# Kernel tuning notes

Hardware: AMD Instinct MI355X
Metric: run time of the kernel (lower is better)

Reference implementation:

```python
import jax, jax.numpy as jnp
import numpy as np
from jax import lax

N, E = 100000, 1600000
IN_DIM, EDGE_DIM, HIDDEN, LAYERS, HEADS, OUT_DIM = 16, 4, 128, 6, 8, 3
C = HIDDEN // HEADS  # per-head dim
EPS = 1e-5


def setup_inputs() -> dict:
    key = jax.random.key(0)
    ks = jax.random.split(key, 24)
    s = 0.1
    inp = {
        "x": jax.random.normal(ks[0], (N, IN_DIM), jnp.float32),
        "edge_index": jax.random.randint(ks[1], (2, E), 0, N, jnp.int32),
        "edge_attr": jax.random.normal(ks[2], (E, EDGE_DIM), jnp.float32),
        # input projection
        "W_in": s * jax.random.normal(ks[3], (IN_DIM, HIDDEN), jnp.float32),
        "b_in": jnp.zeros((HIDDEN,), jnp.float32),
        "ln_in_g": jnp.ones((HIDDEN,), jnp.float32),
        "ln_in_b": jnp.zeros((HIDDEN,), jnp.float32),
        # stacked GAT layer params [L, ...]
        "Wg": s * jax.random.normal(ks[4], (LAYERS, HIDDEN, HIDDEN), jnp.float32),
        "att_src": s * jax.random.normal(ks[5], (LAYERS, HEADS, C), jnp.float32),
        "att_dst": s * jax.random.normal(ks[6], (LAYERS, HEADS, C), jnp.float32),
        "We": s * jax.random.normal(ks[7], (LAYERS, EDGE_DIM, HIDDEN), jnp.float32),
        "att_edge": s * jax.random.normal(ks[8], (LAYERS, HEADS, C), jnp.float32),
        "bg": jnp.zeros((LAYERS, HIDDEN), jnp.float32),
        "ln_g": jnp.ones((LAYERS, HIDDEN), jnp.float32),
        "ln_b": jnp.zeros((LAYERS, HIDDEN), jnp.float32),
        # output head
        "W1": s * jax.random.normal(ks[9], (HIDDEN, HIDDEN), jnp.float32),
        "b1": jnp.zeros((HIDDEN,), jnp.float32),
        "W2": s * jax.random.normal(ks[10], (HIDDEN, OUT_DIM), jnp.float32),
        "b2": jnp.zeros((OUT_DIM,), jnp.float32),
    }
    return inp


def layer_norm(x, g, b):
    mu = jnp.mean(x, axis=-1, keepdims=True)
    var = jnp.var(x, axis=-1, keepdims=True)
    return (x - mu) * lax.rsqrt(var + EPS) * g + b


def gat_block(h, src, dst, edge_attr, Wg, a_s, a_d, We, a_e, bg, g, b):
    # linear projection, shared for src/dst (same input set in PyG GATConv)
    hp = (h @ Wg).reshape(N, HEADS, C)                  # [N,H,C]
    alpha_src = jnp.sum(hp * a_s, axis=-1)              # [N,H]
    alpha_dst = jnp.sum(hp * a_d, axis=-1)              # [N,H]
    ep = (edge_attr @ We).reshape(E, HEADS, C)          # [E,H,C]
    alpha_e = jnp.sum(ep * a_e, axis=-1)                # [E,H]
    # edge-wise attention logits, leaky_relu slope 0.2 (PyG default)
    alpha = jax.nn.leaky_relu(alpha_src[src] + alpha_dst[dst] + alpha_e, 0.2)
    # segment softmax over incoming edges of each dst node
    m = jax.ops.segment_max(alpha, dst, num_segments=N)  # [N,H]
    m = jnp.where(jnp.isfinite(m), m, 0.0)
    a = jnp.exp(alpha - m[dst])
    denom = jax.ops.segment_sum(a, dst, num_segments=N)  # [N,H]
    a = a / (denom[dst] + 1e-16)
    # weighted message aggregation
    msg = hp[src] * a[:, :, None]                        # [E,H,C]
    out = jax.ops.segment_sum(msg, dst, num_segments=N).reshape(N, HIDDEN) + bg
    # residual + LayerNorm (dropout inactive in eval)
    return layer_norm(h + out, g, b)


def reference(x, edge_index, edge_attr, W_in, b_in, ln_in_g, ln_in_b,
              Wg, att_src, att_dst, We, att_edge, bg, ln_g, ln_b,
              W1, b1, W2, b2):
    src, dst = edge_index[0], edge_index[1]
    h = layer_norm(jax.nn.relu(x @ W_in + b_in), ln_in_g, ln_in_b)

    def body(h, p):
        Wg_i, as_i, ad_i, We_i, ae_i, bg_i, g_i, b_i = p
        return gat_block(h, src, dst, edge_attr, Wg_i, as_i, ad_i, We_i, ae_i, bg_i, g_i, b_i), None

    h, _ = lax.scan(body, h, (Wg, att_src, att_dst, We, att_edge, bg, ln_g, ln_b))
    h = jax.nn.relu(h @ W1 + b1)
    return jax.nn.relu(h @ W2 + b2)
```

## Files before the change

kernel.cpp:

```cpp
#include <hip/hip_runtime.h>
#include <hip/hip_bf16.h>

#define NN 100000
#define NE 1600000
#define HID 128
#define NH 8
#define HC 16
#define NL 6
#define CAP 64

typedef unsigned int u32;

__device__ __forceinline__ float u2f(unsigned short v){
  union{u32 i; float f;} c; c.i = ((u32)v) << 16; return c.f;
}
__device__ __forceinline__ float lo2f(u32 u){ union{u32 i; float f;} c; c.i = u << 16; return c.f; }
__device__ __forceinline__ float hi2f(u32 u){ union{u32 i; float f;} c; c.i = u & 0xFFFF0000u; return c.f; }
__device__ __forceinline__ unsigned short f2bf(float f){
  u32 u = __float_as_uint(f);
  u = (u + 0x7FFFu + ((u >> 16) & 1u)) >> 16;
  return (unsigned short)u;
}

__device__ __forceinline__ float ldw(const void* p, long long i, int fl){
  if (fl) return ((const float*)p)[i];
  return u2f(((const unsigned short*)p)[i]);
}

__global__ void sniff_k(const void* g, int* flag){
  if (threadIdx.x == 0 && blockIdx.x == 0){
    const unsigned short* p = (const unsigned short*)g;
    flag[0] = (p[0] == 0x3F80) ? 0 : 1;
  }
}

__global__ void zero_k(int* p, int n){
  int i = blockIdx.x*256 + threadIdx.x;
  if (i < n) p[i] = 0;
}

#define PF_TOT 4355
__global__ void prep_params_k(const void* att_src, const void* att_dst,
    const void* bg, const void* ln_g, const void* ln_b, const void* b1,
    const void* W2, const void* b2, float* __restrict__ pf, const int* flag){
  int fl = flag[0];
  int i = blockIdx.x*256 + threadIdx.x;
  if (i >= PF_TOT) return;
  float v;
  if (i < 768)       v = ldw(att_src, i, fl);
  else if (i < 1536) v = ldw(att_dst, i-768, fl);
  else if (i < 2304) v = ldw(bg, i-1536, fl);
  else if (i < 3072) v = ldw(ln_g, i-2304, fl);
  else if (i < 3840) v = ldw(ln_b, i-3072, fl);
  else if (i < 3968) v = ldw(b1, i-3840, fl);
  else if (i < 4352) v = ldw(W2, i-3968, fl);
  else               v = ldw(b2, i-4352, fl);
  pf[i] = v;
}

__global__ __launch_bounds__(256) void prep_wf_k(const void* Wg, const void* W1,
    float* __restrict__ wF, const int* flag){
  int fl = flag[0];
  long long i = (long long)blockIdx.x*256 + threadIdx.x;
  if (i >= (long long)7*HID*HID) return;
  float v = (i < (long long)6*HID*HID) ? ldw(Wg, i, fl) : ldw(W1, i - (long long)6*HID*HID, fl);
  wF[i] = v;
}

__global__ void prep_wae_k(const void* We, const void* ae, float* __restrict__ Wae,
                           const int* flag){
  int fl = flag[0];
  int id = threadIdx.x;
  if (id >= NL*4*NH) return;
  int l = id / 32, r = id % 32, d = r / 8, hh = r % 8;
  float s = 0.f;
  #pragma unroll
  for (int c = 0; c < HC; ++c)
    s += ldw(We, l*4*HID + d*HID + hh*HC + c, fl) * ldw(ae, l*NH*HC + hh*HC + c, fl);
  Wae[id] = s;
}

__global__ __launch_bounds__(256) void inproj_k(const void* x,
    const void* W_in, const void* b_in, const void* g, const void* b,
    float* __restrict__ h, const int* flag){
  __shared__ float xs[2][16];
  __shared__ float r1[2][2], r2[2][2];
  int fl = flag[0];
  int half = threadIdx.x >> 7;
  int t = threadIdx.x & 127;
  long long n = (long long)blockIdx.x*2 + half;
  if (t < 16) xs[half][t] = ldw(x, n*16 + t, fl);
  __syncthreads();
  float acc = ldw(b_in, t, fl);
  #pragma unroll
  for (int k = 0; k < 16; ++k) acc = fmaf(xs[half][k], ldw(W_in, k*HID + t, fl), acc);
  acc = fmaxf(acc, 0.f);
  float s1 = acc, s2 = acc*acc;
  #pragma unroll
  for (int off = 32; off; off >>= 1){ s1 += __shfl_xor(s1, off); s2 += __shfl_xor(s2, off); }
  if ((t & 63) == 0){ r1[half][t>>6] = s1; r2[half][t>>6] = s2; }
  __syncthreads();
  float S1 = r1[half][0] + r1[half][1], S2 = r2[half][0] + r2[half][1];
  float mu = S1 * (1.f/128.f);
  float var = S2 * (1.f/128.f) - mu*mu;
  float rr = rsqrtf(var + 1e-5f);
  h[n*HID + t] = (acc - mu) * rr * ldw(g, t, fl) + ldw(b, t, fl);
}

__global__ __launch_bounds__(256) void count_k(const int* __restrict__ dst,
    int* __restrict__ deg, int* __restrict__ pos){
  int e = blockIdx.x*256 + threadIdx.x;
  if (e >= NE) return;
  pos[e] = atomicAdd(&deg[dst[e]], 1);
}
__global__ __launch_bounds__(256) void scan_block_k(const int* __restrict__ in,
    int* __restrict__ out, int* __restrict__ bsum, int n){
  __shared__ int lds[256];
  int t = threadIdx.x, i = blockIdx.x*256 + t;
  int v = (i < n) ? in[i] : 0;
  lds[t] = v;
  __syncthreads();
  #pragma unroll
  for (int off = 1; off < 256; off <<= 1){
    int tmp = (t >= off) ? lds[t-off] : 0;
    __syncthreads();
    lds[t] += tmp;
    __syncthreads();
  }
  int incl = lds[t];
  if (i < n) out[i] = incl - v;
  if (t == 255) bsum[blockIdx.x] = incl;
}
__global__ __launch_bounds__(512) void scan_top_k(const int* __restrict__ bsum,
    int* __restrict__ boff, int nb){
  __shared__ int lds[512];
  int t = threadIdx.x;
  int v = (t < nb) ? bsum[t] : 0;
  lds[t] = v;
  __syncthreads();
  #pragma unroll
  for (int off = 1; off < 512; off <<= 1){
    int tmp = (t >= off) ? lds[t-off] : 0;
    __syncthreads();
    lds[t] += tmp;
    __syncthreads();
  }
  boff[t] = lds[t] - v;
}
__global__ __launch_bounds__(256) void scan_add_k(int* __restrict__ rowptr,
    const int* __restrict__ boff, int n){
  int i = blockIdx.x*256 + threadIdx.x;
  if (i < n) rowptr[i] += boff[i >> 8];
  if (i == 0) rowptr[n] = NE;
}
__global__ __launch_bounds__(256) void scatter_k(const int* __restrict__ src,
    const int* __restrict__ dst, const int* __restrict__ rowptr,
    const int* __restrict__ pos, const void* eattr,
    uint4* __restrict__ pk, const int* flag){
  int fl = flag[0];
  int e = blockIdx.x*256 + threadIdx.x;
  if (e >= NE) return;
  int d = dst[e];
  int i = rowptr[d] + pos[e];
  uint4 o;
  o.x = (u32)src[e];
  if (fl){
    float4 v = *(const float4*)((const float*)eattr + (long long)e*4);
    o.y = ((u32)f2bf(v.y) << 16) | (u32)f2bf(v.x);
    o.z = ((u32)f2bf(v.w) << 16) | (u32)f2bf(v.z);
  } else {
    uint2 er = *(const uint2*)((const unsigned short*)eattr + (long long)e*4);
    o.y = er.x; o.z = er.y;
  }
  o.w = 0;
  pk[i] = o;
}

__global__ __launch_bounds__(256) void gemm128_k(const float* __restrict__ A,
    const float* __restrict__ WF, unsigned short* __restrict__ Cout,
    const float* __restrict__ biasF, int relu,
    const float* __restrict__ attS, const float* __restrict__ attD,
    float* __restrict__ asrc, float* __restrict__ adst){
  __shared__ float At[32][132];
  __shared__ float Wt[32][132];
  int t = threadIdx.x;
  int row0 = blockIdx.x * 128;
  int tx = t & 15, ty = t >> 4;
  float acc[8][8] = {};
  for (int k0 = 0; k0 < 128; k0 += 32){
    int ar = t >> 1, ak = (t & 1) * 16;
    float a16[16];
    int arow = row0 + ar;
    if (arow < NN){
      const float* ap = A + (long long)arow*HID + k0 + ak;
      float4 q0 = *(const float4*)ap, q1 = *(const float4*)(ap+4);
      float4 q2 = *(const float4*)(ap+8), q3 = *(const float4*)(ap+12);
      a16[0]=q0.x; a16[1]=q0.y; a16[2]=q0.z; a16[3]=q0.w;
      a16[4]=q1.x; a16[5]=q1.y; a16[6]=q1.z; a16[7]=q1.w;
      a16[8]=q2.x; a16[9]=q2.y; a16[10]=q2.z; a16[11]=q2.w;
      a16[12]=q3.x; a16[13]=q3.y; a16[14]=q3.z; a16[15]=q3.w;
    } else {
      #pragma unroll
      for (int j = 0; j < 16; ++j) a16[j] = 0.f;
    }
    int wk = t >> 3, wn = (t & 7) * 16;
    float w16[16];
    {
      const float* wp = WF + (long long)(k0 + wk)*HID + wn;
      float4 q0 = *(const float4*)wp, q1 = *(const float4*)(wp+4);
      float4 q2 = *(const float4*)(wp+8), q3 = *(const float4*)(wp+12);
      w16[0]=q0.x; w16[1]=q0.y; w16[2]=q0.z; w16[3]=q0.w;
      w16[4]=q1.x; w16[5]=q1.y; w16[6]=q1.z; w16[7]=q1.w;
      w16[8]=q2.x; w16[9]=q2.y; w16[10]=q2.z; w16[11]=q2.w;
      w16[12]=q3.x; w16[13]=q3.y; w16[14]=q3.z; w16[15]=q3.w;
    }
    __syncthreads();
    #pragma unroll
    for (int j = 0; j < 16; ++j) At[ak+j][ar] = a16[j];
    #pragma unroll
    for (int j = 0; j < 16; j += 4){
      float4 q; q.x=w16[j]; q.y=w16[j+1]; q.z=w16[j+2]; q.w=w16[j+3];
      *(float4*)&Wt[wk][wn+j] = q;
    }
    __syncthreads();
    #pragma unroll
    for (int kk = 0; kk < 32; ++kk){
      float4 a0 = *(const float4*)&At[kk][ty*8];
      float4 a1 = *(const float4*)&At[kk][ty*8+4];
      float4 b0 = *(const float4*)&Wt[kk][tx*4];
      float4 b1 = *(const float4*)&Wt[kk][64 + tx*4];
      float am[8] = {a0.x,a0.y,a0.z,a0.w,a1.x,a1.y,a1.z,a1.w};
      float bn[8] = {b0.x,b0.y,b0.z,b0.w,b1.x,b1.y,b1.z,b1.w};
      #pragma unroll
      for (int i2 = 0; i2 < 8; ++i2){
        #pragma unroll
        for (int j2 = 0; j2 < 8; ++j2)
          acc[i2][j2] = fmaf(am[i2], bn[j2], acc[i2][j2]);
      }
    }
  }
  float bb[8];
  #pragma unroll
  for (int j2 = 0; j2 < 8; ++j2){
    int col = (j2 < 4) ? tx*4 + j2 : 64 + tx*4 + (j2 - 4);
    bb[j2] = biasF ? biasF[col] : 0.f;
  }
  #pragma unroll
  for (int i2 = 0; i2 < 8; ++i2){
    int row = row0 + ty*8 + i2;
    if (row < NN){
      float o[8];
      #pragma unroll
      for (int j2 = 0; j2 < 8; ++j2){
        float v = acc[i2][j2] + bb[j2];
        o[j2] = relu ? fmaxf(v, 0.f) : v;
      }
      uint2 p0, p1;
      p0.x = ((u32)f2bf(o[1]) << 16) | (u32)f2bf(o[0]);
      p0.y = ((u32)f2bf(o[3]) << 16) | (u32)f2bf(o[2]);
      p1.x = ((u32)f2bf(o[5]) << 16) | (u32)f2bf(o[4]);
      p1.y = ((u32)f2bf(o[7]) << 16) | (u32)f2bf(o[6]);
      *(uint2*)(Cout + (long long)row*HID + tx*4) = p0;
      *(uint2*)(Cout + (long long)row*HID + 64 + tx*4) = p1;
    }
  }
  if (attS){
    float (*pas)[8][4] = (float (*)[8][4])&At[0][0];
    float (*pad)[8][4] = (float (*)[8][4])&Wt[0][0];
    float avS[8], avD[8];
    #pragma unroll
    for (int j2 = 0; j2 < 8; ++j2){
      int col = (j2 < 4) ? tx*4 + j2 : 64 + tx*4 + (j2 - 4);
      avS[j2] = attS[col]; avD[j2] = attD[col];
    }
    int h0 = tx >> 2, slot = tx & 3;
    __syncthreads();
    #pragma unroll
    for (int i2 = 0; i2 < 8; ++i2){
      float ps0 = 0.f, pd0 = 0.f, ps1 = 0.f, pd1 = 0.f;
      #pragma unroll
      for (int j2 = 0; j2 < 4; ++j2){
        ps0 = fmaf(acc[i2][j2],   avS[j2],   ps0);
        pd0 = fmaf(acc[i2][j2],   avD[j2],   pd0);
        ps1 = fmaf(acc[i2][j2+4], avS[j2+4], ps1);
        pd1 = fmaf(acc[i2][j2+4], avD[j2+4], pd1);
      }
      int row = ty*8 + i2;
      pas[row][h0][slot] = ps0;   pad[row][h0][slot] = pd0;
      pas[row][h0+4][slot] = ps1; pad[row][h0+4][slot] = pd1;
    }
    __syncthreads();
    #pragma unroll
    for (int q = 0; q < 4; ++q){
      int idx = t + 256*q;
      int row = idx >> 3, hh = idx & 7;
      int rr = row0 + row;
      if (rr < NN){
        asrc[(long long)rr*NH + hh] = pas[row][hh][0] + pas[row][hh][1]
                                    + pas[row][hh][2] + pas[row][hh][3];
        adst[(long long)rr*NH + hh] = pad[row][hh][0] + pad[row][hh][1]
                                    + pad[row][hh][2] + pad[row][hh][3];
      }
    }
  }
}

__global__ __launch_bounds__(256) void gat_node_k(const int* __restrict__ rowptr,
    const uint4* __restrict__ pk,
    const float* __restrict__ Wae_l, const float* __restrict__ asrc,
    const float* __restrict__ adst, const unsigned short* __restrict__ hp,
    float* __restrict__ h, const float* __restrict__ bgF,
    const float* __restrict__ gF, const float* __restrict__ bF){
  __shared__ float lw[4][CAP][8];
  __shared__ int   ls[4][CAP];
  int wv = threadIdx.x >> 6, l = threadIdx.x & 63;
  int n = blockIdx.x*4 + wv;
  int b0 = rowptr[n], b1 = rowptr[n+1];
  int deg = b1 - b0;
  int sub = l >> 3, hh = l & 7;
  float wae0 = Wae_l[hh], wae1 = Wae_l[8+hh], wae2 = Wae_l[16+hh], wae3 = Wae_l[24+hh];
  float adn = adst[n*NH + hh];
  float den = 0.f;
  for (int i = b0 + sub; i < b1; i += 8){
    uint4 q = pk[i];
    int s = (int)q.x;
    float v = asrc[s*NH + hh] + adn;
    v = fmaf(lo2f(q.y), wae0, v);
    v = fmaf(hi2f(q.y), wae1, v);
    v = fmaf(lo2f(q.z), wae2, v);
    v = fmaf(hi2f(q.z), wae3, v);
    v = fmaxf(v, 0.2f*v);
    float w = __expf(v);
    int idx = i - b0;
    if (idx < CAP){
      lw[wv][idx][hh] = w;
      if (hh == 0) ls[wv][idx] = s;
    }
    den += w;
  }
  den += __shfl_xor(den, 8);
  den += __shfl_xor(den, 16);
  den += __shfl_xor(den, 32);
  int eg = l >> 4, cl = l & 15;
  int hd = cl >> 1;
  float rden = 1.f / (__shfl(den, hd) + 1e-16f);
  const unsigned short* hpc = hp + 8*cl;
  float a[8] = {0,0,0,0,0,0,0,0};
  int cap_end = b0 + (deg < CAP ? deg : CAP);
  int i = b0;
  for (; i + 8 <= cap_end; i += 8){
    int j0 = i + eg, j1 = i + 4 + eg;
    int s0 = ls[wv][j0 - b0], s1v = ls[wv][j1 - b0];
    float w0 = lw[wv][j0 - b0][hd], w1 = lw[wv][j1 - b0][hd];
    uint4 q0 = *(const uint4*)(hpc + (long long)s0*HID);
    uint4 q1 = *(const uint4*)(hpc + (long long)s1v*HID);
    a[0] = fmaf(w0, lo2f(q0.x), a[0]); a[1] = fmaf(w0, hi2f(q0.x), a[1]);
    a[2] = fmaf(w0, lo2f(q0.y), a[2]); a[3] = fmaf(w0, hi2f(q0.y), a[3]);
    a[4] = fmaf(w0, lo2f(q0.z), a[4]); a[5] = fmaf(w0, hi2f(q0.z), a[5]);
    a[6] = fmaf(w0, lo2f(q0.w), a[6]); a[7] = fmaf(w0, hi2f(q0.w), a[7]);
    a[0] = fmaf(w1, lo2f(q1.x), a[0]); a[1] = fmaf(w1, hi2f(q1.x), a[1]);
    a[2] = fmaf(w1, lo2f(q1.y), a[2]); a[3] = fmaf(w1, hi2f(q1.y), a[3]);
    a[4] = fmaf(w1, lo2f(q1.z), a[4]); a[5] = fmaf(w1, hi2f(q1.z), a[5]);
    a[6] = fmaf(w1, lo2f(q1.w), a[6]); a[7] = fmaf(w1, hi2f(q1.w), a[7]);
  }
  for (; i < cap_end; i += 4){
    int j = i + eg;
    if (j < cap_end){
      int s = ls[wv][j - b0];
      float w = lw[wv][j - b0][hd];
      uint4 q = *(const uint4*)(hpc + (long long)s*HID);
      a[0] = fmaf(w, lo2f(q.x), a[0]); a[1] = fmaf(w, hi2f(q.x), a[1]);
      a[2] = fmaf(w, lo2f(q.y), a[2]); a[3] = fmaf(w, hi2f(q.y), a[3]);
      a[4] = fmaf(w, lo2f(q.z), a[4]); a[5] = fmaf(w, hi2f(q.z), a[5]);
      a[6] = fmaf(w, lo2f(q.w), a[6]); a[7] = fmaf(w, hi2f(q.w), a[7]);
    }
  }
  if (deg > CAP){
    float w0c = Wae_l[hd], w1c = Wae_l[8+hd], w2c = Wae_l[16+hd], w3c = Wae_l[24+hd];
    float adc = adst[n*NH + hd];
    for (int j = cap_end + eg; j < b1; j += 4){
      uint4 e4 = pk[j];
      int s = (int)e4.x;
      float v = asrc[s*NH + hd] + adc;
      v = fmaf(lo2f(e4.y), w0c, v);
      v = fmaf(hi2f(e4.y), w1c, v);
      v = fmaf(lo2f(e4.z), w2c, v);
      v = fmaf(hi2f(e4.z), w3c, v);
      v = fmaxf(v, 0.2f*v);
      float w = __expf(v);
      uint4 q = *(const uint4*)(hpc + (long long)s*HID);
      a[0] = fmaf(w, lo2f(q.x), a[0]); a[1] = fmaf(w, hi2f(q.x), a[1]);
      a[2] = fmaf(w, lo2f(q.y), a[2]); a[3] = fmaf(w, hi2f(q.y), a[3]);
      a[4] = fmaf(w, lo2f(q.z), a[4]); a[5] = fmaf(w, hi2f(q.z), a[5]);
      a[6] = fmaf(w, lo2f(q.w), a[6]); a[7] = fmaf(w, hi2f(q.w), a[7]);
    }
  }
  #pragma unroll
  for (int j = 0; j < 8; ++j){
    a[j] += __shfl_xor(a[j], 16);
    a[j] += __shfl_xor(a[j], 32);
  }
  const float* hrow = h + (long long)n*HID + 8*cl;
  float4 hv0 = *(const float4*)hrow;
  float4 hv1 = *(const float4*)(hrow + 4);
  float hv[8] = {hv0.x,hv0.y,hv0.z,hv0.w,hv1.x,hv1.y,hv1.z,hv1.w};
  float tv[8];
  float s1 = 0.f, s2 = 0.f;
  #pragma unroll
  for (int j = 0; j < 8; ++j){
    tv[j] = hv[j] + a[j]*rden + bgF[8*cl + j];
    s1 += tv[j]; s2 += tv[j]*tv[j];
  }
  s1 += __shfl_xor(s1, 1); s2 += __shfl_xor(s2, 1);
  s1 += __shfl_xor(s1, 2); s2 += __shfl_xor(s2, 2);
  s1 += __shfl_xor(s1, 4); s2 += __shfl_xor(s2, 4);
  s1 += __shfl_xor(s1, 8); s2 += __shfl_xor(s2, 8);
  float mu = s1 * (1.f/128.f);
  float var = s2 * (1.f/128.f) - mu*mu;
  float rr = rsqrtf(var + 1e-5f);
  if (eg == 0){
    float4 o0, o1;
    o0.x = (tv[0]-mu)*rr*gF[8*cl+0] + bF[8*cl+0];
    o0.y = (tv[1]-mu)*rr*gF[8*cl+1] + bF[8*cl+1];
    o0.z = (tv[2]-mu)*rr*gF[8*cl+2] + bF[8*cl+2];
    o0.w = (tv[3]-mu)*rr*gF[8*cl+3] + bF[8*cl+3];
    o1.x = (tv[4]-mu)*rr*gF[8*cl+4] + bF[8*cl+4];
    o1.y = (tv[5]-mu)*rr*gF[8*cl+5] + bF[8*cl+5];
    o1.z = (tv[6]-mu)*rr*gF[8*cl+6] + bF[8*cl+6];
    o1.w = (tv[7]-mu)*rr*gF[8*cl+7] + bF[8*cl+7];
    *(float4*)(h + (long long)n*HID + 8*cl) = o0;
    *(float4*)(h + (long long)n*HID + 8*cl + 4) = o1;
  }
}

__global__ __launch_bounds__(256) void head2_k(const unsigned short* __restrict__ hp,
    const float* __restrict__ W2F, const float* __restrict__ b2F, void* out,
    const int* flag){
  int fl = flag[0];
  int n = blockIdx.x*4 + (threadIdx.x >> 6);
  if (n >= NN) return;
  int l = threadIdx.x & 63;
  u32 u = *(const u32*)(hp + (long long)n*HID + 2*l);
  float p0 = lo2f(u), p1 = hi2f(u);
  int c0 = 2*l, c1 = 2*l + 1;
  float o0 = p0*W2F[c0*3+0] + p1*W2F[c1*3+0];
  float o1 = p0*W2F[c0*3+1] + p1*W2F[c1*3+1];
  float o2 = p0*W2F[c0*3+2] + p1*W2F[c1*3+2];
  #pragma unroll
  for (int off = 32; off; off >>= 1){
    o0 += __shfl_xor(o0, off); o1 += __shfl_xor(o1, off); o2 += __shfl_xor(o2, off);
  }
  if (l == 0){
    float r0 = fmaxf(o0 + b2F[0], 0.f);
    float r1 = fmaxf(o1 + b2F[1], 0.f);
    float r2 = fmaxf(o2 + b2F[2], 0.f);
    if (fl){
      float* o = (float*)out;
      o[n*3+0] = r0; o[n*3+1] = r1; o[n*3+2] = r2;
    } else {
      unsigned short* o = (unsigned short*)out;
      o[n*3+0] = f2bf(r0); o[n*3+1] = f2bf(r1); o[n*3+2] = f2bf(r2);
    }
  }
}

extern "C" void kernel_launch(void* const* d_in, const int* in_sizes, int n_in,
                              void* d_out, int out_size, void* d_ws, size_t ws_size,
                              hipStream_t stream){
  const void* x       = d_in[0];
  const int*  eidx    = (const int*)d_in[1];
  const void* eattr   = d_in[2];
  const void* W_in    = d_in[3];
  const void* b_in    = d_in[4];
  const void* ln_in_g = d_in[5];
  const void* ln_in_b = d_in[6];
  const void* Wg      = d_in[7];
  const void* att_src = d_in[8];
  const void* att_dst = d_in[9];
  const void* We      = d_in[10];
  const void* att_e   = d_in[11];
  const void* bg      = d_in[12];
  const void* ln_g    = d_in[13];
  const void* ln_b    = d_in[14];
  const void* W1      = d_in[15];
  const void* b1v     = d_in[16];
  const void* W2      = d_in[17];
  const void* b2      = d_in[18];

  char* ws = (char*)d_ws;
  size_t off = 0;
  auto alloc = [&](size_t bytes) -> void* {
    void* p = ws + off; off += (bytes + 255) & ~(size_t)255; return p;
  };
  float*  h     = (float*) alloc((size_t)NN*HID*4);
  unsigned short* hp = (unsigned short*)alloc((size_t)NN*HID*2);
  float*  asrc  = (float*) alloc((size_t)NN*NH*4);
  float*  adst  = (float*) alloc((size_t)NN*NH*4);
  float*  Wae   = (float*) alloc(NL*32*4);
  float*  pf    = (float*) alloc(PF_TOT*4);
  float*  wF    = (float*) alloc((size_t)7*HID*HID*4);
  int* deg      = (int*)   alloc((size_t)NN*4);
  int* pos      = (int*)   alloc((size_t)NE*4);
  int* rowptr   = (int*)   alloc((size_t)(NN+1)*4);
  int* bsum     = (int*)   alloc(512*4);
  int* boffp    = (int*)   alloc(512*4);
  uint4* pk     = (uint4*) alloc((size_t)NE*16);
  int* flag     = (int*)   alloc(256);

  const int* src = eidx;
  const int* dst = eidx + NE;
  int nb = (NN + 255) / 256;

  sniff_k<<<1, 64, 0, stream>>>(ln_in_g, flag);
  zero_k<<<nb, 256, 0, stream>>>(deg, NN);
  prep_wae_k<<<1, 256, 0, stream>>>(We, att_e, Wae, flag);
  prep_params_k<<<(PF_TOT+255)/256, 256, 0, stream>>>(att_src, att_dst, bg, ln_g, ln_b,
                                                      b1v, W2, b2, pf, flag);
  prep_wf_k<<<(7*HID*HID+255)/256, 256, 0, stream>>>(Wg, W1, wF, flag);
  inproj_k<<<NN/2, 256, 0, stream>>>(x, W_in, b_in, ln_in_g, ln_in_b, h, flag);
  count_k<<<(NE+255)/256, 256, 0, stream>>>(dst, deg, pos);
  scan_block_k<<<nb, 256, 0, stream>>>(deg, rowptr, bsum, NN);
  scan_top_k<<<1, 512, 0, stream>>>(bsum, boffp, nb);
  scan_add_k<<<nb, 256, 0, stream>>>(rowptr, boffp, NN);
  scatter_k<<<(NE+255)/256, 256, 0, stream>>>(src, dst, rowptr, pos, eattr, pk, flag);

  const float* attS = pf;
  const float* attD = pf + 768;
  const float* bgF  = pf + 1536;
  const float* gF   = pf + 2304;
  const float* bF   = pf + 3072;
  const float* b1F  = pf + 3840;
  const float* W2F  = pf + 3968;
  const float* b2F  = pf + 4352;

  int gblocks = (NN + 127) / 128;
  for (int l = 0; l < NL; ++l){
    gemm128_k<<<gblocks, 256, 0, stream>>>(h, wF + (size_t)l*HID*HID, hp,
                                           nullptr, 0, attS + l*128, attD + l*128,
                                           asrc, adst);
    gat_node_k<<<NN/4, 256, 0, stream>>>(rowptr, pk, Wae + l*32, asrc, adst,
                                         hp, h, bgF + l*128, gF + l*128, bF + l*128);
  }
  gemm128_k<<<gblocks, 256, 0, stream>>>(h, wF + (size_t)6*HID*HID, hp, b1F, 1,
                                         nullptr, nullptr, nullptr, nullptr);
  head2_k<<<(NN+3)/4, 256, 0, stream>>>(hp, W2F, b2F, d_out, flag);
}
```

Baseline: 1.278 ms.

## Replace FP32 SIMT GEMM with bf16 MFMA GEMM using swizzled LDS tiles

The per-layer 128x128 node projection GEMM moves from FP32 FMA on the vector ALUs to v_mfma_f32_16x16x32_bf16 matrix instructions. Weights are pre-transposed, cast to bf16 and XOR-swizzled once in a prep kernel. Activations are cast to bf16 while being staged into LDS. The epilogue stages the bf16 output through LDS for coalesced stores, and the attention dot products are now computed from the rounded bf16 outputs. This cuts GEMM compute time and weight bandwidth, at the cost of bf16 rounding of the inputs and of the attention-logit source.

```diff
diff --git a/kernel.cpp b/kernel.cpp
--- a/kernel.cpp
+++ b/kernel.cpp
@@ -10,6 +10,8 @@
 #define CAP 64
 
 typedef unsigned int u32;
+typedef __attribute__((ext_vector_type(4))) float f32x4;
+typedef __attribute__((ext_vector_type(8))) short bf16x8;
 
 __device__ __forceinline__ float u2f(unsigned short v){
   union{u32 i; float f;} c; c.i = ((u32)v) << 16; return c.f;
@@ -58,13 +60,17 @@
   pf[i] = v;
 }
 
-__global__ __launch_bounds__(256) void prep_wf_k(const void* Wg, const void* W1,
-    float* __restrict__ wF, const int* flag){
+__global__ __launch_bounds__(256) void prep_wb_k(const void* Wg, const void* W1,
+    unsigned short* __restrict__ wB, const int* flag){
   int fl = flag[0];
-  long long i = (long long)blockIdx.x*256 + threadIdx.x;
-  if (i >= (long long)7*HID*HID) return;
-  float v = (i < (long long)6*HID*HID) ? ldw(Wg, i, fl) : ldw(W1, i - (long long)6*HID*HID, fl);
-  wF[i] = v;
+  int i = blockIdx.x*256 + threadIdx.x;
+  if (i >= 7*HID*HID) return;
+  int l = i >> 14, r = i & 16383;
+  int n = r >> 7, k = r & 127;
+  float v = (l < 6) ? ldw(Wg, (long long)l*HID*HID + k*HID + n, fl)
+                    : ldw(W1, (long long)k*HID + n, fl);
+  int ks = (((k >> 3) ^ (n & 7)) << 3) | (k & 7);
+  wB[(long long)l*HID*HID + n*HID + ks] = f2bf(v);
 }
 
 __global__ void prep_wae_k(const void* We, const void* ae, float* __restrict__ Wae,
@@ -176,130 +182,130 @@
   pk[i] = o;
 }
 
-__global__ __launch_bounds__(256) void gemm128_k(const float* __restrict__ A,
-    const float* __restrict__ WF, unsigned short* __restrict__ Cout,
+__global__ __launch_bounds__(256) void gemm_mfma_k(const float* __restrict__ A,
+    const unsigned short* __restrict__ wBl, unsigned short* __restrict__ Cout,
     const float* __restrict__ biasF, int relu,
     const float* __restrict__ attS, const float* __restrict__ attD,
     float* __restrict__ asrc, float* __restrict__ adst){
-  __shared__ float At[32][132];
-  __shared__ float Wt[32][132];
+  __shared__ unsigned short smem[2*HID*HID];
+  unsigned short* As = smem;
+  unsigned short* Bs = smem + HID*HID;
   int t = threadIdx.x;
   int row0 = blockIdx.x * 128;
-  int tx = t & 15, ty = t >> 4;
-  float acc[8][8] = {};
-  for (int k0 = 0; k0 < 128; k0 += 32){
-    int ar = t >> 1, ak = (t & 1) * 16;
-    float a16[16];
-    int arow = row0 + ar;
+
+  {
+    const uint4* srcp = (const uint4*)wBl;
+    uint4* dstp = (uint4*)Bs;
+    #pragma unroll
+    for (int i = 0; i < 8; ++i) dstp[i*256 + t] = srcp[i*256 + t];
+  }
+  {
+    int r = t >> 1, kh = (t & 1) * 64;
+    int arow = row0 + r;
+    float a64[64];
     if (arow < NN){
-      const float* ap = A + (long long)arow*HID + k0 + ak;
-      float4 q0 = *(const float4*)ap, q1 = *(const float4*)(ap+4);
-      float4 q2 = *(const float4*)(ap+8), q3 = *(const float4*)(ap+12);
-      a16[0]=q0.x; a16[1]=q0.y; a16[2]=q0.z; a16[3]=q0.w;
-      a16[4]=q1.x; a16[5]=q1.y; a16[6]=q1.z; a16[7]=q1.w;
-      a16[8]=q2.x; a16[9]=q2.y; a16[10]=q2.z; a16[11]=q2.w;
-      a16[12]=q3.x; a16[13]=q3.y; a16[14]=q3.z; a16[15]=q3.w;
+      const float* ap = A + (long long)arow*HID + kh;
+      #pragma unroll
+      for (int i = 0; i < 16; ++i){
+        float4 q = *(const float4*)(ap + 4*i);
+        a64[4*i] = q.x; a64[4*i+1] = q.y; a64[4*i+2] = q.z; a64[4*i+3] = q.w;
+      }
     } else {
       #pragma unroll
-      for (int j = 0; j < 16; ++j) a16[j] = 0.f;
-    }
-    int wk = t >> 3, wn = (t & 7) * 16;
-    float w16[16];
-    {
-      const float* wp = WF + (long long)(k0 + wk)*HID + wn;
-      float4 q0 = *(const float4*)wp, q1 = *(const float4*)(wp+4);
-      float4 q2 = *(const float4*)(wp+8), q3 = *(const float4*)(wp+12);
-      w16[0]=q0.x; w16[1]=q0.y; w16[2]=q0.z; w16[3]=q0.w;
-      w16[4]=q1.x; w16[5]=q1.y; w16[6]=q1.z; w16[7]=q1.w;
-      w16[8]=q2.x; w16[9]=q2.y; w16[10]=q2.z; w16[11]=q2.w;
-      w16[12]=q3.x; w16[13]=q3.y; w16[14]=q3.z; w16[15]=q3.w;
-    }
-    __syncthreads();
-    #pragma unroll
-    for (int j = 0; j < 16; ++j) At[ak+j][ar] = a16[j];
-    #pragma unroll
-    for (int j = 0; j < 16; j += 4){
-      float4 q; q.x=w16[j]; q.y=w16[j+1]; q.z=w16[j+2]; q.w=w16[j+3];
-      *(float4*)&Wt[wk][wn+j] = q;
-    }
-    __syncthreads();
-    #pragma unroll
-    for (int kk = 0; kk < 32; ++kk){
-      float4 a0 = *(const float4*)&At[kk][ty*8];
-      float4 a1 = *(const float4*)&At[kk][ty*8+4];
-      float4 b0 = *(const float4*)&Wt[kk][tx*4];
-      float4 b1 = *(const float4*)&Wt[kk][64 + tx*4];
-      float am[8] = {a0.x,a0.y,a0.z,a0.w,a1.x,a1.y,a1.z,a1.w};
-      float bn[8] = {b0.x,b0.y,b0.z,b0.w,b1.x,b1.y,b1.z,b1.w};
+      for (int i = 0; i < 64; ++i) a64[i] = 0.f;
+    }
+    #pragma unroll
+    for (int g = 0; g < 8; ++g){
+      int gg = (kh >> 3) + g;
+      u32 wp[4];
       #pragma unroll
-      for (int i2 = 0; i2 < 8; ++i2){
+      for (int p = 0; p < 4; ++p)
+        wp[p] = ((u32)f2bf(a64[g*8 + 2*p + 1]) << 16) | (u32)f2bf(a64[g*8 + 2*p]);
+      uint4 q; q.x = wp[0]; q.y = wp[1]; q.z = wp[2]; q.w = wp[3];
+      *(uint4*)&As[r*HID + ((gg ^ (r & 7)) << 3)] = q;
+    }
+  }
+  __syncthreads();
+
+  int l = t & 63, wv = t >> 6;
+  int wr = wv >> 1, wc = wv & 1;
+  int lr = l & 15, lg = l >> 4;
+  f32x4 acc[4][4] = {};
+  #pragma unroll
+  for (int kk = 0; kk < 4; ++kk){
+    bf16x8 af[4], bfr[4];
+    int grp = kk*4 + lg;
+    #pragma unroll
+    for (int m = 0; m < 4; ++m){
+      int row = wr*64 + m*16 + lr;
+      af[m] = *(const bf16x8*)&As[row*HID + ((grp ^ (row & 7)) << 3)];
+    }
+    #pragma unroll
+    for (int n = 0; n < 4; ++n){
+      int col = wc*64 + n*16 + lr;
+      bfr[n] = *(const bf16x8*)&Bs[col*HID + ((grp ^ (col & 7)) << 3)];
+    }
+    #pragma unroll
+    for (int m = 0; m < 4; ++m){
+      #pragma unroll
+      for (int n = 0; n < 4; ++n){
+        asm volatile("v_mfma_f32_16x16x32_bf16 %0, %1, %2, %0"
+                     : "+v"(acc[m][n]) : "v"(af[m]), "v"(bfr[n]));
+      }
+    }
+  }
+  __syncthreads();
+
+  unsigned short* Cl = smem;
+  #pragma unroll
+  for (int m = 0; m < 4; ++m){
+    #pragma unroll
+    for (int n = 0; n < 4; ++n){
+      int col = wc*64 + n*16 + lr;
+      float bv = biasF ? biasF[col] : 0.f;
+      #pragma unroll
+      for (int j = 0; j < 4; ++j){
+        int row = wr*64 + m*16 + lg*4 + j;
+        float v = acc[m][n][j] + bv;
+        if (relu) v = fmaxf(v, 0.f);
+        Cl[row*136 + col] = f2bf(v);
+      }
+    }
+  }
+  __syncthreads();
+
+  {
+    int r = t >> 1, kh = (t & 1)*64;
+    if (row0 + r < NN){
+      const uint4* srcp = (const uint4*)&Cl[r*136 + kh];
+      uint4* dstp = (uint4*)(Cout + (long long)(row0 + r)*HID + kh);
+      #pragma unroll
+      for (int i = 0; i < 8; ++i) dstp[i] = srcp[i];
+    }
+  }
+  if (attS){
+    int hh = t & 7;
+    float avS[16], avD[16];
+    #pragma unroll
+    for (int c = 0; c < 16; ++c){ avS[c] = attS[hh*16 + c]; avD[c] = attD[hh*16 + c]; }
+    #pragma unroll
+    for (int q = 0; q < 4; ++q){
+      int r = q*32 + (t >> 3);
+      int rr = row0 + r;
+      if (rr < NN){
+        const unsigned short* cp = &Cl[r*136 + hh*16];
+        uint4 q0 = *(const uint4*)cp;
+        uint4 q1 = *(const uint4*)(cp + 8);
+        u32 uu[8] = {q0.x,q0.y,q0.z,q0.w,q1.x,q1.y,q1.z,q1.w};
+        float sS = 0.f, sD = 0.f;
         #pragma unroll
-        for (int j2 = 0; j2 < 8; ++j2)
-          acc[i2][j2] = fmaf(am[i2], bn[j2], acc[i2][j2]);
-      }
-    }
-  }
-  float bb[8];
-  #pragma unroll
-  for (int j2 = 0; j2 < 8; ++j2){
-    int col = (j2 < 4) ? tx*4 + j2 : 64 + tx*4 + (j2 - 4);
-    bb[j2] = biasF ? biasF[col] : 0.f;
-  }
-  #pragma unroll
-  for (int i2 = 0; i2 < 8; ++i2){
-    int row = row0 + ty*8 + i2;
-    if (row < NN){
-      float o[8];
-      #pragma unroll
-      for (int j2 = 0; j2 < 8; ++j2){
-        float v = acc[i2][j2] + bb[j2];
-        o[j2] = relu ? fmaxf(v, 0.f) : v;
-      }
-      uint2 p0, p1;
-      p0.x = ((u32)f2bf(o[1]) << 16) | (u32)f2bf(o[0]);
-      p0.y = ((u32)f2bf(o[3]) << 16) | (u32)f2bf(o[2]);
-      p1.x = ((u32)f2bf(o[5]) << 16) | (u32)f2bf(o[4]);
-      p1.y = ((u32)f2bf(o[7]) << 16) | (u32)f2bf(o[6]);
-      *(uint2*)(Cout + (long long)row*HID + tx*4) = p0;
-      *(uint2*)(Cout + (long long)row*HID + 64 + tx*4) = p1;
-    }
-  }
-  if (attS){
-    float (*pas)[8][4] = (float (*)[8][4])&At[0][0];
-    float (*pad)[8][4] = (float (*)[8][4])&Wt[0][0];
-    float avS[8], avD[8];
-    #pragma unroll
-    for (int j2 = 0; j2 < 8; ++j2){
-      int col = (j2 < 4) ? tx*4 + j2 : 64 + tx*4 + (j2 - 4);
-      avS[j2] = attS[col]; avD[j2] = attD[col];
-    }
-    int h0 = tx >> 2, slot = tx & 3;
-    __syncthreads();
-    #pragma unroll
-    for (int i2 = 0; i2 < 8; ++i2){
-      float ps0 = 0.f, pd0 = 0.f, ps1 = 0.f, pd1 = 0.f;
-      #pragma unroll
-      for (int j2 = 0; j2 < 4; ++j2){
-        ps0 = fmaf(acc[i2][j2],   avS[j2],   ps0);
-        pd0 = fmaf(acc[i2][j2],   avD[j2],   pd0);
-        ps1 = fmaf(acc[i2][j2+4], avS[j2+4], ps1);
-        pd1 = fmaf(acc[i2][j2+4], avD[j2+4], pd1);
-      }
-      int row = ty*8 + i2;
-      pas[row][h0][slot] = ps0;   pad[row][h0][slot] = pd0;
-      pas[row][h0+4][slot] = ps1; pad[row][h0+4][slot] = pd1;
-    }
-    __syncthreads();
-    #pragma unroll
-    for (int q = 0; q < 4; ++q){
-      int idx = t + 256*q;
-      int row = idx >> 3, hh = idx & 7;
-      int rr = row0 + row;
-      if (rr < NN){
-        asrc[(long long)rr*NH + hh] = pas[row][hh][0] + pas[row][hh][1]
-                                    + pas[row][hh][2] + pas[row][hh][3];
-        adst[(long long)rr*NH + hh] = pad[row][hh][0] + pad[row][hh][1]
-                                    + pad[row][hh][2] + pad[row][hh][3];
+        for (int p = 0; p < 8; ++p){
+          float h0 = lo2f(uu[p]), h1 = hi2f(uu[p]);
+          sS = fmaf(h0, avS[2*p], sS); sS = fmaf(h1, avS[2*p+1], sS);
+          sD = fmaf(h0, avD[2*p], sD); sD = fmaf(h1, avD[2*p+1], sD);
+        }
+        asrc[(long long)rr*NH + hh] = sS;
+        adst[(long long)rr*NH + hh] = sD;
       }
     }
   }
@@ -498,7 +504,7 @@
   float*  adst  = (float*) alloc((size_t)NN*NH*4);
   float*  Wae   = (float*) alloc(NL*32*4);
   float*  pf    = (float*) alloc(PF_TOT*4);
-  float*  wF    = (float*) alloc((size_t)7*HID*HID*4);
+  unsigned short* wB = (unsigned short*)alloc((size_t)7*HID*HID*2);
   int* deg      = (int*)   alloc((size_t)NN*4);
   int* pos      = (int*)   alloc((size_t)NE*4);
   int* rowptr   = (int*)   alloc((size_t)(NN+1)*4);
@@ -516,7 +522,7 @@
   prep_wae_k<<<1, 256, 0, stream>>>(We, att_e, Wae, flag);
   prep_params_k<<<(PF_TOT+255)/256, 256, 0, stream>>>(att_src, att_dst, bg, ln_g, ln_b,
                                                       b1v, W2, b2, pf, flag);
-  prep_wf_k<<<(7*HID*HID+255)/256, 256, 0, stream>>>(Wg, W1, wF, flag);
+  prep_wb_k<<<(7*HID*HID+255)/256, 256, 0, stream>>>(Wg, W1, wB, flag);
   inproj_k<<<NN/2, 256, 0, stream>>>(x, W_in, b_in, ln_in_g, ln_in_b, h, flag);
   count_k<<<(NE+255)/256, 256, 0, stream>>>(dst, deg, pos);
   scan_block_k<<<nb, 256, 0, stream>>>(deg, rowptr, bsum, NN);
@@ -535,13 +541,13 @@
 
   int gblocks = (NN + 127) / 128;
   for (int l = 0; l < NL; ++l){
-    gemm128_k<<<gblocks, 256, 0, stream>>>(h, wF + (size_t)l*HID*HID, hp,
-                                           nullptr, 0, attS + l*128, attD + l*128,
-                                           asrc, adst);
+    gemm_mfma_k<<<gblocks, 256, 0, stream>>>(h, wB + (size_t)l*HID*HID, hp,
+                                             nullptr, 0, attS + l*128, attD + l*128,
+                                             asrc, adst);
     gat_node_k<<<NN/4, 256, 0, stream>>>(rowptr, pk, Wae + l*32, asrc, adst,
                                          hp, h, bgF + l*128, gF + l*128, bF + l*128);
   }
-  gemm128_k<<<gblocks, 256, 0, stream>>>(h, wF + (size_t)6*HID*HID, hp, b1F, 1,
-                                         nullptr, nullptr, nullptr, nullptr);
+  gemm_mfma_k<<<gblocks, 256, 0, stream>>>(h, wB + (size_t)6*HID*HID, hp, b1F, 1,
+                                           nullptr, nullptr, nullptr, nullptr);
   head2_k<<<(NN+3)/4, 256, 0, stream>>>(hp, W2F, b2F, d_out, flag);
 }
```

New measurement: 1.049 ms. 1.22x faster.
